# Performance work log

Measured on AMD Instinct MI355X. Metric: run time of the kernel, lower is better.

The kernel has to match this reference:

```python
import jax, jax.numpy as jnp
import numpy as np

RADIUS = 1.0
N_NORM = 1  # default n_norm in the torch module


def setup_inputs() -> dict:
    key = jax.random.key(0)
    k1, k2, k3 = jax.random.split(key, 3)
    batch, n, c_in, c_out = 8, 2048, 64, 64
    features = jax.random.normal(k1, (batch, n, c_in), dtype=jnp.float32)
    geometry = jax.random.normal(k2, (batch, n, 3), dtype=jnp.float32)
    # learned per-edge kernel weight: K(diff)[o,i] = sum_x diff[x] * Wk[x,o,i]
    Wk = jax.random.normal(k3, (3, c_out, c_in), dtype=jnp.float32) * 0.1
    return {"features": features, "geometry": geometry, "Wk": Wk}


def reference(features, geometry, Wk):
    # diff[z,a,b,:] = geometry[z,b] - geometry[z,a]   (rb - ra in the torch code)
    diff = geometry[:, None, :, :] - geometry[:, :, None, :]  # [z, a, b, 3]
    norm = jnp.sqrt(jnp.sum(diff * diff, axis=-1))            # [z, a, b]
    # Dense masked formulation: padding every point's neighbor list to k = n
    # with rel_mask zeros is mathematically identical to the torch variable-k
    # padding (masked entries contribute nothing to the einsum reduce).
    rel_mask = (norm < RADIUS).astype(features.dtype)         # [z, a, b]
    # Fused reduce. Original: einsum('zab,zabij,zabj->zai', mask, K(diff), feat[nei])
    # with K(diff)[z,a,b,i,j] = einsum('zabx,xij->zabij', diff, Wk). We contract
    # over b first to avoid materializing the [z,a,b,i,j] kernel tensor.
    s = jnp.einsum('zab,zabx,zbj->zaxj', rel_mask, diff, features)  # [z, a, 3, c_in]
    out = jnp.einsum('zaxj,xij->zai', s, Wk) / jnp.sqrt(jnp.asarray(N_NORM, features.dtype))
    return out
```

## Files before the change

kernel.cpp:

```cpp
#include <hip/hip_runtime.h>
#include <stdint.h>

#define NPTS 2048

#define BP_OFF    0ULL
#define BP_BYTES  (8ULL * 16 * 64 * 1024)
#define W2F_OFF   (BP_OFF + BP_BYTES)
#define W2F_BYTES (24ULL * 1024)
#define WXF_OFF   (W2F_OFF + W2F_BYTES)
#define WXF_BYTES (24ULL * 1024)
#define MW_OFF    (WXF_OFF + WXF_BYTES)
#define MW_BYTES  (8ULL * 32 * 64 * 256)

typedef __attribute__((ext_vector_type(8))) short bf16x8;
typedef __attribute__((ext_vector_type(4))) float f32x4;
typedef __attribute__((ext_vector_type(4))) unsigned int u32x4;

__device__ __forceinline__ unsigned f2bf(float f) {
  union { float f; unsigned u; } v; v.f = f;
  return (v.u + 0x7FFFu + ((v.u >> 16) & 1u)) >> 16;
}

__device__ __forceinline__ bf16x8 pack8(const float4 a, const float4 b) {
  u32x4 r;
  r[0] = f2bf(a.x) | (f2bf(a.y) << 16);
  r[1] = f2bf(a.z) | (f2bf(a.w) << 16);
  r[2] = f2bf(b.x) | (f2bf(b.y) << 16);
  r[3] = f2bf(b.z) | (f2bf(b.w) << 16);
  union { u32x4 u; bf16x8 h; } c; c.u = r; return c.h;
}

__device__ __forceinline__ bf16x8 unpack_mask(unsigned mq) {
  const unsigned dep0 = ((mq & 15u) * 0x204081u) & 0x01010101u;
  const unsigned dep1 = (((mq >> 4) & 15u) * 0x204081u) & 0x01010101u;
  u32x4 aw;
  aw[0] = __builtin_amdgcn_perm(dep0, 0u, 0x0C050C04u) * 0x3F80u;
  aw[1] = __builtin_amdgcn_perm(dep0, 0u, 0x0C070C06u) * 0x3F80u;
  aw[2] = __builtin_amdgcn_perm(dep1, 0u, 0x0C050C04u) * 0x3F80u;
  aw[3] = __builtin_amdgcn_perm(dep1, 0u, 0x0C070C06u) * 0x3F80u;
  union { u32x4 u; bf16x8 h; } cv; cv.u = aw;
  return cv.h;
}

__global__ __launch_bounds__(256, 2) void k1_prep(const float* __restrict__ feat,
                                                  const float* __restrict__ geom,
                                                  const float* __restrict__ Wk,
                                                  unsigned char* __restrict__ ws) {
  const int blk = blockIdx.x, t = threadIdx.x;
  if (blk < 512) {
    const int z = blk >> 6, s = blk & 63;
    __shared__ float FT[64][37];
    __shared__ float g[96];
    __shared__ float gxp[2048], gyp[2048], gzp[2048];
    const float* fz = feat + ((size_t)z * NPTS + s * 32) * 64;
    const float* gz = geom + (size_t)z * NPTS * 3;
    {
      const int row = t >> 3, j0 = (t & 7) << 3;
      const float4 v0 = *(const float4*)&fz[row * 64 + j0];
      const float4 v1 = *(const float4*)&fz[row * 64 + j0 + 4];
      FT[j0 + 0][row] = v0.x; FT[j0 + 1][row] = v0.y;
      FT[j0 + 2][row] = v0.z; FT[j0 + 3][row] = v0.w;
      FT[j0 + 4][row] = v1.x; FT[j0 + 5][row] = v1.y;
      FT[j0 + 6][row] = v1.z; FT[j0 + 7][row] = v1.w;
    }
    if (t < 96) g[t] = gz[s * 96 + t];
    {
      float v[24];
#pragma unroll
      for (int i = 0; i < 6; ++i) *(float4*)&v[i * 4] = *(const float4*)&gz[t * 24 + i * 4];
#pragma unroll
      for (int i = 0; i < 8; ++i) {
        const int pp = i * 256 + t;
        gxp[pp] = v[i * 3 + 0]; gyp[pp] = v[i * 3 + 1]; gzp[pp] = v[i * 3 + 2];
      }
    }
    __syncthreads();

    {
      const int w = t >> 6, L = t & 63;
      const int nn = L >> 2, k0 = (L & 3) * 8;
      const int j = w * 16 + nn;
      float f[8];
#pragma unroll
      for (int i = 0; i < 8; ++i) f[i] = FT[j][k0 + i];
      float gx[3][8];
#pragma unroll
      for (int x = 0; x < 3; ++x)
#pragma unroll
        for (int i = 0; i < 8; ++i) gx[x][i] = g[(k0 + i) * 3 + x];
      unsigned char* base = ws + BP_OFF + (size_t)z * 1048576 + (size_t)w * 65536 +
                            (size_t)s * 1024 + L * 16;
#pragma unroll
      for (int it = 0; it < 4; ++it) {
        u32x4 pv;
#pragma unroll
        for (int p = 0; p < 4; ++p) {
          float f0 = f[2 * p], f1 = f[2 * p + 1];
          if (it < 3) { f0 *= gx[it][2 * p]; f1 *= gx[it][2 * p + 1]; }
          pv[p] = f2bf(f0) | (f2bf(f1) << 16);
        }
        *(u32x4*)(base + (size_t)it * 4 * 65536) = pv;
      }
    }

    {
      float ax[8], ay[8], az[8];
#pragma unroll
      for (int i = 0; i < 8; ++i) {
        const int pp = i * 256 + t;
        ax[i] = gxp[pp]; ay[i] = gyp[pp]; az[i] = gzp[pp];
      }
      unsigned bits[8] = {0, 0, 0, 0, 0, 0, 0, 0};
      for (int j = 0; j < 32; ++j) {
        const float bx = g[j * 3 + 0], by = g[j * 3 + 1], bz = g[j * 3 + 2];
#pragma unroll
        for (int i = 0; i < 8; ++i) {
          const float d0 = bx - ax[i], d1 = by - ay[i], d2 = bz - az[i];
          const float n2 = fmaf(d2, d2, fmaf(d1, d1, d0 * d0));
          bits[i] |= (n2 < 1.0f ? 1u : 0u) << j;
        }
      }
      unsigned int* mw = (unsigned int*)(ws + MW_OFF);
#pragma unroll
      for (int i = 0; i < 8; ++i) {
        const int r = t * 8 + i;
        mw[(((size_t)z * 32 + (r >> 6)) * 64 + s) * 64 + (r & 15) * 4 + ((r >> 4) & 3)] = bits[i];
      }
    }
  } else if (blk == 512) {
    for (int e = t; e < 1536; e += 256) {
      const int frag = e >> 6, lp = e & 63, nn = lp >> 2, qd = lp & 3;
      const int kb = frag >> 2, cb = frag & 3;
      u32x4 pv;
#pragma unroll
      for (int p = 0; p < 4; ++p) {
        const int k0 = kb * 32 + qd * 8 + 2 * p;
        const float v0 = Wk[(k0 >> 6) * 4096 + (cb * 16 + nn) * 64 + (k0 & 63)];
        const float v1 = Wk[((k0 + 1) >> 6) * 4096 + (cb * 16 + nn) * 64 + ((k0 + 1) & 63)];
        pv[p] = f2bf(v0) | (f2bf(v1) << 16);
      }
      *(u32x4*)(ws + W2F_OFF + (size_t)frag * 1024 + lp * 16) = pv;
    }
  } else {
    for (int e = t; e < 1536; e += 256) {
      const int frag = e >> 6, lp = e & 63, nn = lp >> 2, qd = lp & 3;
      const int kb = frag / 12, cb = frag % 12, xi = cb * 16 + nn;
      u32x4 pv;
#pragma unroll
      for (int p = 0; p < 4; ++p) {
        const int k0 = kb * 32 + qd * 8 + 2 * p;
        const float v0 = Wk[(xi >> 6) * 4096 + (xi & 63) * 64 + k0];
        const float v1 = Wk[(xi >> 6) * 4096 + (xi & 63) * 64 + k0 + 1];
        pv[p] = f2bf(v0) | (f2bf(v1) << 16);
      }
      *(u32x4*)(ws + WXF_OFF + (size_t)frag * 1024 + lp * 16) = pv;
    }
  }
}

__global__ __launch_bounds__(512, 2) void k2_gemm(const float* __restrict__ geom,
                                                  const unsigned char* __restrict__ ws,
                                                  float* __restrict__ out) {
  __shared__ __align__(16) float Ct[64 * 256];

  const int t = threadIdx.x, lane = t & 63, w = t >> 6;
  const int quad = (lane >> 4) & 3, n = lane & 15;
  const int bx = blockIdx.x;
  const int z = bx & 7, at = bx >> 3, a0 = at * 64;
  const int fragoff = n * 64 + quad * 16;
  const int qsh = quad * 8;

  const unsigned char* bpz = ws + BP_OFF + (size_t)z * 1048576 + (size_t)(2 * w) * 65536;
  const unsigned char* mwz = ws + MW_OFF + ((size_t)z * 32 + at) * 16384;

  f32x4 acc[4][2];
#pragma unroll
  for (int rg = 0; rg < 4; ++rg)
#pragma unroll
    for (int cb = 0; cb < 2; ++cb)
#pragma unroll
      for (int r = 0; r < 4; ++r) acc[rg][cb][r] = 0.f;

  bf16x8 Bf[4][2];
  u32x4 Mf[4];
#pragma unroll
  for (int sl = 0; sl < 4; ++sl) {
#pragma unroll
    for (int cb = 0; cb < 2; ++cb)
      Bf[sl][cb] = *(const bf16x8*)(bpz + (size_t)cb * 65536 + (size_t)sl * 1024 + fragoff);
    Mf[sl] = *(const u32x4*)(mwz + sl * 256 + n * 16);
  }

#define KSTEP(S, SL)                                                           \
  {                                                                            \
    const u32x4 mw = Mf[SL];                                                   \
    _Pragma("unroll") for (int rg = 0; rg < 4; ++rg) {                         \
      const bf16x8 Af = unpack_mask((mw[rg] >> qsh) & 0xFFu);                  \
      _Pragma("unroll") for (int cb = 0; cb < 2; ++cb)                         \
        acc[rg][cb] = __builtin_amdgcn_mfma_f32_16x16x32_bf16(                 \
            Af, Bf[SL][cb], acc[rg][cb], 0, 0, 0);                             \
    }                                                                          \
    const int sp = (S) + 4 > 63 ? 63 : (S) + 4;                                \
    Mf[SL] = *(const u32x4*)(mwz + sp * 256 + n * 16);                         \
    _Pragma("unroll") for (int cb = 0; cb < 2; ++cb)                           \
      Bf[SL][cb] = *(const bf16x8*)(bpz + (size_t)cb * 65536 +                 \
                                    (size_t)sp * 1024 + fragoff);              \
  }

  for (int s4 = 0; s4 < 64; s4 += 4) {
    KSTEP(s4 + 0, 0) KSTEP(s4 + 1, 1) KSTEP(s4 + 2, 2) KSTEP(s4 + 3, 3)
  }
#undef KSTEP

#pragma unroll
  for (int rg = 0; rg < 4; ++rg)
#pragma unroll
    for (int cb = 0; cb < 2; ++cb)
#pragma unroll
      for (int r = 0; r < 4; ++r) {
        const int row = rg * 16 + quad * 4 + r;
        const int col = 32 * w + cb * 16 + n;
        Ct[row * 256 + (((col >> 2) ^ row) << 2) + (col & 3)] = acc[rg][cb][r];
      }
  __syncthreads();

  if (w < 4) {
    const int lm = 16 * w + n;
    bf16x8 Across[8];
#pragma unroll
    for (int kb = 0; kb < 8; ++kb) {
      const int c0 = (kb * 8 + quad * 2) ^ lm;
      const int c1 = (kb * 8 + quad * 2 + 1) ^ lm;
      const float4 f0 = *(const float4*)&Ct[lm * 256 + c0 * 4];
      const float4 f1 = *(const float4*)&Ct[lm * 256 + c1 * 4];
      Across[kb] = pack8(f0, f1);
    }

    f32x4 mn[4], V[12];
#pragma unroll
    for (int i = 0; i < 4; ++i)
#pragma unroll
      for (int r = 0; r < 4; ++r) mn[i][r] = 0.f;
#pragma unroll
    for (int i = 0; i < 12; ++i)
#pragma unroll
      for (int r = 0; r < 4; ++r) V[i][r] = 0.f;

    const unsigned char* w2f = ws + W2F_OFF;
    const unsigned char* wxf = ws + WXF_OFF;
#pragma unroll
    for (int kb = 0; kb < 6; ++kb)
#pragma unroll
      for (int cb = 0; cb < 4; ++cb) {
        const bf16x8 Bfr = *(const bf16x8*)(w2f + (size_t)(kb * 4 + cb) * 1024 + fragoff);
        mn[cb] = __builtin_amdgcn_mfma_f32_16x16x32_bf16(Across[kb], Bfr, mn[cb], 0, 0, 0);
      }
#pragma unroll
    for (int kb = 0; kb < 2; ++kb)
#pragma unroll
      for (int cb = 0; cb < 12; ++cb) {
        const bf16x8 Bfr = *(const bf16x8*)(wxf + (size_t)(kb * 12 + cb) * 1024 + fragoff);
        V[cb] = __builtin_amdgcn_mfma_f32_16x16x32_bf16(Across[6 + kb], Bfr, V[cb], 0, 0, 0);
      }

#pragma unroll
    for (int r = 0; r < 4; ++r) {
      const int af = a0 + 16 * w + quad * 4 + r;
      const float g0 = geom[((size_t)z * NPTS + af) * 3 + 0];
      const float g1 = geom[((size_t)z * NPTS + af) * 3 + 1];
      const float g2 = geom[((size_t)z * NPTS + af) * 3 + 2];
#pragma unroll
      for (int cb = 0; cb < 4; ++cb) {
        const float v = mn[cb][r] - g0 * V[cb][r] - g1 * V[cb + 4][r] - g2 * V[cb + 8][r];
        out[((size_t)z * NPTS + af) * 64 + cb * 16 + n] = v;
      }
    }
  }
}

extern "C" void kernel_launch(void* const* d_in, const int* in_sizes, int n_in,
                              void* d_out, int out_size, void* d_ws, size_t ws_size,
                              hipStream_t stream) {
  const float* feat = (const float*)d_in[0];
  const float* geom = (const float*)d_in[1];
  const float* Wk   = (const float*)d_in[2];
  float* out = (float*)d_out;
  unsigned char* ws = (unsigned char*)d_ws;

  k1_prep<<<dim3(514), 256, 0, stream>>>(feat, geom, Wk, ws);
  k2_gemm<<<dim3(256), 512, 0, stream>>>(geom, ws, out);
}
```

Measured before the change: 102.9 us.

## Split the GEMM tile across 16 waves with halved per-wave row work

Doubles the k2_gemm block from 512 to 1024 threads. Each wave now computes 32 rows by 32 columns instead of 64 rows by 32 columns, loading only half of the packed mask words. The aim is more resident waves per CU to hide the global-load latency of the streamed B fragments and masks, with fewer accumulators per wave. In exchange, B fragments are loaded twice across the wave pair, and the tighter launch bounds may pressure registers. The prefetch now reads a few slices past the end of the loop instead of clamping.

Measured after the change: 119.2 us. +15.9%, slower.

```diff
diff --git a/kernel.cpp b/kernel.cpp
--- a/kernel.cpp
+++ b/kernel.cpp
@@ -15,6 +15,7 @@
 typedef __attribute__((ext_vector_type(8))) short bf16x8;
 typedef __attribute__((ext_vector_type(4))) float f32x4;
 typedef __attribute__((ext_vector_type(4))) unsigned int u32x4;
+typedef __attribute__((ext_vector_type(2))) unsigned int u32x2;
 
 __device__ __forceinline__ unsigned f2bf(float f) {
   union { float f; unsigned u; } v; v.f = f;
@@ -158,9 +159,9 @@
   }
 }
 
-__global__ __launch_bounds__(512, 2) void k2_gemm(const float* __restrict__ geom,
-                                                  const unsigned char* __restrict__ ws,
-                                                  float* __restrict__ out) {
+__global__ __launch_bounds__(1024, 4) void k2_gemm(const float* __restrict__ geom,
+                                                   const unsigned char* __restrict__ ws,
+                                                   float* __restrict__ out) {
   __shared__ __align__(16) float Ct[64 * 256];
 
   const int t = threadIdx.x, lane = t & 63, w = t >> 6;
@@ -169,57 +170,62 @@
   const int z = bx & 7, at = bx >> 3, a0 = at * 64;
   const int fragoff = n * 64 + quad * 16;
   const int qsh = quad * 8;
-
-  const unsigned char* bpz = ws + BP_OFF + (size_t)z * 1048576 + (size_t)(2 * w) * 65536;
-  const unsigned char* mwz = ws + MW_OFF + ((size_t)z * 32 + at) * 16384;
-
-  f32x4 acc[4][2];
-#pragma unroll
-  for (int rg = 0; rg < 4; ++rg)
+  const int h = w & 1, c = w >> 1;
+
+  const unsigned char* bp0 = ws + BP_OFF + (size_t)z * 1048576 +
+                             (size_t)(2 * c) * 65536 + fragoff;
+  const unsigned char* bp1 = bp0 + 65536;
+  const unsigned char* mp = ws + MW_OFF + ((size_t)z * 32 + at) * 16384 + n * 16 + 8 * h;
+
+  f32x4 acc[2][2];
+#pragma unroll
+  for (int rg = 0; rg < 2; ++rg)
 #pragma unroll
     for (int cb = 0; cb < 2; ++cb)
 #pragma unroll
       for (int r = 0; r < 4; ++r) acc[rg][cb][r] = 0.f;
 
   bf16x8 Bf[4][2];
-  u32x4 Mf[4];
+  u32x2 Mf[4];
 #pragma unroll
   for (int sl = 0; sl < 4; ++sl) {
+    Bf[sl][0] = *(const bf16x8*)(bp0 + sl * 1024);
+    Bf[sl][1] = *(const bf16x8*)(bp1 + sl * 1024);
+    Mf[sl] = *(const u32x2*)(mp + sl * 256);
+  }
+
+#define KSTEP(SL)                                                              \
+  {                                                                            \
+    const u32x2 mw = Mf[SL];                                                   \
+    const bf16x8 Af0 = unpack_mask(mw[0] >> qsh);                              \
+    const bf16x8 Af1 = unpack_mask(mw[1] >> qsh);                              \
+    acc[0][0] = __builtin_amdgcn_mfma_f32_16x16x32_bf16(Af0, Bf[SL][0],        \
+                                                        acc[0][0], 0, 0, 0);   \
+    acc[0][1] = __builtin_amdgcn_mfma_f32_16x16x32_bf16(Af0, Bf[SL][1],        \
+                                                        acc[0][1], 0, 0, 0);   \
+    acc[1][0] = __builtin_amdgcn_mfma_f32_16x16x32_bf16(Af1, Bf[SL][0],        \
+                                                        acc[1][0], 0, 0, 0);   \
+    acc[1][1] = __builtin_amdgcn_mfma_f32_16x16x32_bf16(Af1, Bf[SL][1],        \
+                                                        acc[1][1], 0, 0, 0);   \
+    Mf[SL] = *(const u32x2*)(mp + SL * 256);                                   \
+    Bf[SL][0] = *(const bf16x8*)(bp0 + SL * 1024);                             \
+    Bf[SL][1] = *(const bf16x8*)(bp1 + SL * 1024);                             \
+  }
+
+  for (int s4 = 0; s4 < 64; s4 += 4) {
+    bp0 += 4096; bp1 += 4096; mp += 1024;
+    KSTEP(0) KSTEP(1) KSTEP(2) KSTEP(3)
+  }
+#undef KSTEP
+
+#pragma unroll
+  for (int rg = 0; rg < 2; ++rg)
 #pragma unroll
     for (int cb = 0; cb < 2; ++cb)
-      Bf[sl][cb] = *(const bf16x8*)(bpz + (size_t)cb * 65536 + (size_t)sl * 1024 + fragoff);
-    Mf[sl] = *(const u32x4*)(mwz + sl * 256 + n * 16);
-  }
-
-#define KSTEP(S, SL)                                                           \
-  {                                                                            \
-    const u32x4 mw = Mf[SL];                                                   \
-    _Pragma("unroll") for (int rg = 0; rg < 4; ++rg) {                         \
-      const bf16x8 Af = unpack_mask((mw[rg] >> qsh) & 0xFFu);                  \
-      _Pragma("unroll") for (int cb = 0; cb < 2; ++cb)                         \
-        acc[rg][cb] = __builtin_amdgcn_mfma_f32_16x16x32_bf16(                 \
-            Af, Bf[SL][cb], acc[rg][cb], 0, 0, 0);                             \
-    }                                                                          \
-    const int sp = (S) + 4 > 63 ? 63 : (S) + 4;                                \
-    Mf[SL] = *(const u32x4*)(mwz + sp * 256 + n * 16);                         \
-    _Pragma("unroll") for (int cb = 0; cb < 2; ++cb)                           \
-      Bf[SL][cb] = *(const bf16x8*)(bpz + (size_t)cb * 65536 +                 \
-                                    (size_t)sp * 1024 + fragoff);              \
-  }
-
-  for (int s4 = 0; s4 < 64; s4 += 4) {
-    KSTEP(s4 + 0, 0) KSTEP(s4 + 1, 1) KSTEP(s4 + 2, 2) KSTEP(s4 + 3, 3)
-  }
-#undef KSTEP
-
-#pragma unroll
-  for (int rg = 0; rg < 4; ++rg)
-#pragma unroll
-    for (int cb = 0; cb < 2; ++cb)
 #pragma unroll
       for (int r = 0; r < 4; ++r) {
-        const int row = rg * 16 + quad * 4 + r;
-        const int col = 32 * w + cb * 16 + n;
+        const int row = 32 * h + rg * 16 + quad * 4 + r;
+        const int col = (2 * c + cb) * 16 + n;
         Ct[row * 256 + (((col >> 2) ^ row) << 2) + (col & 3)] = acc[rg][cb][r];
       }
   __syncthreads();
@@ -288,5 +294,5 @@
   unsigned char* ws = (unsigned char*)d_ws;
 
   k1_prep<<<dim3(514), 256, 0, stream>>>(feat, geom, Wk, ws);
-  k2_gemm<<<dim3(256), 512, 0, stream>>>(geom, ws, out);
-}
+  k2_gemm<<<dim3(256), 1024, 0, stream>>>(geom, ws, out);
+}
```
